# Kernel optimization log

Measured on AMD Instinct MI355X. Metric: run time of the kernel, lower is better.

Reference implementation:

```python
import jax, jax.numpy as jnp
import numpy as np

NUM_FIELDS = 40
EMBED_DIM = 64
ATTN_DIM = 32

def _triu_index(n):
    i, j = np.triu_indices(n, k=1)
    return jnp.asarray(i, jnp.int32), jnp.asarray(j, jnp.int32)

def setup_inputs() -> dict:
    key = jax.random.key(0)
    k0, k1, k2, k3, k4, k5 = jax.random.split(key, 6)
    B = 8192
    inputs = jax.random.normal(k0, (B, NUM_FIELDS, EMBED_DIM), dtype=jnp.float32)
    # attention MLP params (PyTorch Linear default init scale ~ 1/sqrt(fan_in))
    s1 = 1.0 / np.sqrt(EMBED_DIM)
    s2 = 1.0 / np.sqrt(ATTN_DIM)
    W1 = jax.random.uniform(k1, (EMBED_DIM, ATTN_DIM), jnp.float32, -s1, s1)
    b1 = jax.random.uniform(k2, (ATTN_DIM,), jnp.float32, -s1, s1)
    w2 = jax.random.uniform(k3, (ATTN_DIM,), jnp.float32, -s2, s2)
    p = jax.random.uniform(k4, (EMBED_DIM,), jnp.float32, -s1, s1)
    return {"inputs": inputs, "W1": W1, "b1": b1, "w2": w2, "p": p}

def reference(inputs, W1, b1, w2, p):
    idx0, idx1 = _triu_index(NUM_FIELDS)  # [P], P = 780 pairs
    # gather pairwise field embeddings and take elementwise product: [B, P, D]
    prod = inputs[:, idx0, :] * inputs[:, idx1, :]
    # tiny attention MLP: Linear -> ReLU -> Linear(no bias) -> softmax over pairs
    h = jax.nn.relu(jnp.einsum('bpd,da->bpa', prod, W1) + b1)  # [B, P, A]
    logits = jnp.einsum('bpa,a->bp', h, w2)                    # [B, P]
    attn = jax.nn.softmax(logits, axis=1)                      # softmax over pair dim
    # attention-weighted sum pooling over pairs: [B, D]
    pooled = jnp.einsum('bp,bpd->bd', attn, prod)
    # final linear projection to scalar (dropout=0 / eval -> identity)
    return jnp.einsum('bd,d->b', pooled, p)
```

## Files before the change

### kernel.cpp

```cpp
#include <hip/hip_runtime.h>


typedef _Float16 f16;
typedef f16 f16x2 __attribute__((ext_vector_type(2)));
typedef f16 f16x4 __attribute__((ext_vector_type(4)));
typedef f16 f16x8 __attribute__((ext_vector_type(8)));
typedef float fx16 __attribute__((ext_vector_type(16)));

#define NF 40
#define NB 8192
#define STR 76

union V8 { f16x8 v8; f16x4 v4[2]; f16x2 v2[4]; };

__global__ __launch_bounds__(256, 4) void afm_kernel(
    const float* __restrict__ x,
    const float* __restrict__ W1,
    const float* __restrict__ b1,
    const float* __restrict__ w2,
    const float* __restrict__ p,
    float* __restrict__ out)
{
    __shared__ f16 xh[4][NF * STR];

    const int tid  = threadIdx.x;
    const int wid  = tid >> 6;
    const int lane = tid & 63;
    const int b    = blockIdx.x * 4 + wid;

    f16* Xs = &xh[wid][0];

    const float4* xb = (const float4*)(x + (size_t)b * (NF * 64));
#pragma unroll
    for (int t = 0; t < 5; ++t) {
        int g = t * 64 + lane;
        float4 v0 = xb[g * 2];
        float4 v1 = xb[g * 2 + 1];
        f16x4 lo = { (f16)v0.x, (f16)v0.y, (f16)v0.z, (f16)v0.w };
        f16x4 hi = { (f16)v1.x, (f16)v1.y, (f16)v1.z, (f16)v1.w };
        int row = g >> 3, gg = g & 7;
        f16* dst = Xs + row * STR + gg * 8;
        *(f16x4*)dst = lo;
        *(f16x4*)(dst + 4) = hi;
    }

    const int nl = lane & 31;
    const int hh = lane >> 5;
    const int h8 = hh * 8;

    f16x8 w1f[4];
#pragma unroll
    for (int kt = 0; kt < 4; ++kt)
#pragma unroll
        for (int j = 0; j < 8; ++j)
            w1f[kt][j] = (f16)W1[(kt * 16 + h8 + j) * 32 + nl];

    f16x2 pp[16];
#pragma unroll
    for (int kt = 0; kt < 4; ++kt)
#pragma unroll
        for (int m = 0; m < 4; ++m) {
            f16x2 t2 = { (f16)p[kt * 16 + h8 + 2 * m], (f16)p[kt * 16 + h8 + 2 * m + 1] };
            pp[kt * 4 + m] = t2;
        }

    fx16 b1C;
    f16x2 w2h[8];
#pragma unroll
    for (int r = 0; r < 16; ++r) {
        int a = (r & 3) + 8 * (r >> 2) + 4 * hh;
        b1C[r] = b1[a];
    }
#pragma unroll
    for (int m = 0; m < 8; ++m) {
        int r = 2 * m;
        int a = (r & 3) + 8 * (r >> 2) + 4 * hh;
        f16x2 t2 = { (f16)(w2[a] * 1.44269504f), (f16)(w2[a + 1] * 1.44269504f) };
        w2h[m] = t2;
    }

    f16x4 xif[8];
    {
        const f16* src = Xs + nl * STR + h8;
#pragma unroll
        for (int kt = 0; kt < 4; ++kt) {
            xif[2 * kt]     = *(const f16x4*)(src + kt * 16);
            xif[2 * kt + 1] = *(const f16x4*)(src + kt * 16 + 4);
        }
    }

    float accW = 0.f, accWS = 0.f;

    auto body = [&](const f16x4* xi, int jrow, bool valid) {
        const f16* base = Xs + jrow * STR + h8;
        V8 pr[4];
#pragma unroll
        for (int kt = 0; kt < 4; ++kt) {
            f16x4 a0 = *(const f16x4*)(base + kt * 16);
            f16x4 a1 = *(const f16x4*)(base + kt * 16 + 4);
            pr[kt].v4[0] = xi[2 * kt] * a0;
            pr[kt].v4[1] = xi[2 * kt + 1] * a1;
        }
        fx16 C = __builtin_amdgcn_mfma_f32_32x32x16_f16(w1f[0], pr[0].v8, b1C, 0, 0, 0);
        C = __builtin_amdgcn_mfma_f32_32x32x16_f16(w1f[1], pr[1].v8, C, 0, 0, 0);
        C = __builtin_amdgcn_mfma_f32_32x32x16_f16(w1f[2], pr[2].v8, C, 0, 0, 0);
        C = __builtin_amdgcn_mfma_f32_32x32x16_f16(w1f[3], pr[3].v8, C, 0, 0, 0);
        float s0 = 0.f, s1 = 0.f, s2 = 0.f, s3 = 0.f;
#pragma unroll
        for (int m = 0; m < 4; ++m) {
            s0 = __builtin_amdgcn_fdot2(pr[0].v2[m], pp[m],      s0, false);
            s1 = __builtin_amdgcn_fdot2(pr[1].v2[m], pp[4 + m],  s1, false);
            s2 = __builtin_amdgcn_fdot2(pr[2].v2[m], pp[8 + m],  s2, false);
            s3 = __builtin_amdgcn_fdot2(pr[3].v2[m], pp[12 + m], s3, false);
        }
        float sp = (s0 + s1) + (s2 + s3);
        const f16x2 z2 = { (f16)0.f, (f16)0.f };
        float l0 = 0.f, l1 = 0.f;
#pragma unroll
        for (int m = 0; m < 8; ++m) {
            f16x2 hm = __builtin_bit_cast(f16x2,
                __builtin_amdgcn_cvt_pkrtz(C[2 * m], C[2 * m + 1]));
            hm = __builtin_elementwise_max(hm, z2);
            if (m & 1) l1 = __builtin_amdgcn_fdot2(hm, w2h[m], l1, false);
            else       l0 = __builtin_amdgcn_fdot2(hm, w2h[m], l0, false);
        }
        float l = l0 + l1;
        l  += __shfl_xor(l, 32);
        sp += __shfl_xor(sp, 32);
        float w = __builtin_amdgcn_exp2f(l);
        if (!valid) w = 0.f;
        accW += w;
        accWS = fmaf(w, sp, accWS);
    };

    for (int t = 1; t <= 24; ++t) {
        int jrow = (t <= 16) ? ((nl + t) & 31) : (t + 15);
        bool valid = (t != 16) || (nl < 16);
        body(xif, jrow, valid);
    }
    {
        int q = nl < 28 ? nl : 27;
        float disc = 225.0f - 8.0f * (float)q;
        int ii = (int)((15.0f - sqrtf(disc)) * 0.5f);
        if (ii * (15 - ii) / 2 > q) --ii;
        if ((ii + 1) * (14 - ii) / 2 <= q) ++ii;
        int jj = q - ii * (15 - ii) / 2 + ii + 1;
        int iC = 32 + ii, jC = 32 + jj;
        f16x4 xi2[8];
        const f16* src = Xs + iC * STR + h8;
#pragma unroll
        for (int kt = 0; kt < 4; ++kt) {
            xi2[2 * kt]     = *(const f16x4*)(src + kt * 16);
            xi2[2 * kt + 1] = *(const f16x4*)(src + kt * 16 + 4);
        }
        body(xi2, jC, nl < 28);
    }

#pragma unroll
    for (int m = 16; m >= 1; m >>= 1) {
        accW  += __shfl_xor(accW, m);
        accWS += __shfl_xor(accWS, m);
    }
    if (lane == 0) out[b] = accWS / accW;
}

extern "C" void kernel_launch(void* const* d_in, const int* in_sizes, int n_in,
                              void* d_out, int out_size, void* d_ws, size_t ws_size,
                              hipStream_t stream) {
    const float* x  = (const float*)d_in[0];
    const float* W1 = (const float*)d_in[1];
    const float* b1 = (const float*)d_in[2];
    const float* w2 = (const float*)d_in[3];
    const float* p  = (const float*)d_in[4];
    float* out = (float*)d_out;
    dim3 grid(NB / 4), block(256);
    hipLaunchKernelGGL(afm_kernel, grid, block, 0, stream, x, W1, b1, w2, p, out);
}
```

Measured before the change: 150.1 us.

## Split MFMA accumulation chain, pre-scale xi by p, defer sp shuffle

```diff
diff --git a/kernel.cpp b/kernel.cpp
--- a/kernel.cpp
+++ b/kernel.cpp
@@ -55,21 +55,12 @@
         for (int j = 0; j < 8; ++j)
             w1f[kt][j] = (f16)W1[(kt * 16 + h8 + j) * 32 + nl];
 
-    f16x2 pp[16];
-#pragma unroll
-    for (int kt = 0; kt < 4; ++kt)
-#pragma unroll
-        for (int m = 0; m < 4; ++m) {
-            f16x2 t2 = { (f16)p[kt * 16 + h8 + 2 * m], (f16)p[kt * 16 + h8 + 2 * m + 1] };
-            pp[kt * 4 + m] = t2;
-        }
-
-    fx16 b1C;
+    fx16 b1h;
     f16x2 w2h[8];
 #pragma unroll
     for (int r = 0; r < 16; ++r) {
         int a = (r & 3) + 8 * (r >> 2) + 4 * hh;
-        b1C[r] = b1[a];
+        b1h[r] = 0.5f * b1[a];
     }
 #pragma unroll
     for (int m = 0; m < 8; ++m) {
@@ -88,45 +79,54 @@
             xif[2 * kt + 1] = *(const f16x4*)(src + kt * 16 + 4);
         }
     }
+    f16x2 xip[16];
+#pragma unroll
+    for (int kt = 0; kt < 4; ++kt) {
+        V8 u; u.v4[0] = xif[2 * kt]; u.v4[1] = xif[2 * kt + 1];
+#pragma unroll
+        for (int m = 0; m < 4; ++m) {
+            f16x2 pe = { (f16)p[kt * 16 + h8 + 2 * m], (f16)p[kt * 16 + h8 + 2 * m + 1] };
+            xip[kt * 4 + m] = u.v2[m] * pe;
+        }
+    }
 
     float accW = 0.f, accWS = 0.f;
 
-    auto body = [&](const f16x4* xi, int jrow, bool valid) {
+    auto body = [&](const f16x4* xi, const f16x2* xp, int jrow, bool valid) {
         const f16* base = Xs + jrow * STR + h8;
-        V8 pr[4];
+        float s[4];
+        fx16 Ca, Cb;
 #pragma unroll
         for (int kt = 0; kt < 4; ++kt) {
-            f16x4 a0 = *(const f16x4*)(base + kt * 16);
-            f16x4 a1 = *(const f16x4*)(base + kt * 16 + 4);
-            pr[kt].v4[0] = xi[2 * kt] * a0;
-            pr[kt].v4[1] = xi[2 * kt + 1] * a1;
+            V8 xj;
+            xj.v4[0] = *(const f16x4*)(base + kt * 16);
+            xj.v4[1] = *(const f16x4*)(base + kt * 16 + 4);
+            float sk = 0.f;
+#pragma unroll
+            for (int m = 0; m < 4; ++m)
+                sk = __builtin_amdgcn_fdot2(xj.v2[m], xp[kt * 4 + m], sk, false);
+            s[kt] = sk;
+            V8 pr;
+            pr.v4[0] = xi[2 * kt] * xj.v4[0];
+            pr.v4[1] = xi[2 * kt + 1] * xj.v4[1];
+            if (kt == 0)      Ca = __builtin_amdgcn_mfma_f32_32x32x16_f16(w1f[0], pr.v8, b1h, 0, 0, 0);
+            else if (kt == 1) Ca = __builtin_amdgcn_mfma_f32_32x32x16_f16(w1f[1], pr.v8, Ca,  0, 0, 0);
+            else if (kt == 2) Cb = __builtin_amdgcn_mfma_f32_32x32x16_f16(w1f[2], pr.v8, b1h, 0, 0, 0);
+            else              Cb = __builtin_amdgcn_mfma_f32_32x32x16_f16(w1f[3], pr.v8, Cb,  0, 0, 0);
         }
-        fx16 C = __builtin_amdgcn_mfma_f32_32x32x16_f16(w1f[0], pr[0].v8, b1C, 0, 0, 0);
-        C = __builtin_amdgcn_mfma_f32_32x32x16_f16(w1f[1], pr[1].v8, C, 0, 0, 0);
-        C = __builtin_amdgcn_mfma_f32_32x32x16_f16(w1f[2], pr[2].v8, C, 0, 0, 0);
-        C = __builtin_amdgcn_mfma_f32_32x32x16_f16(w1f[3], pr[3].v8, C, 0, 0, 0);
-        float s0 = 0.f, s1 = 0.f, s2 = 0.f, s3 = 0.f;
-#pragma unroll
-        for (int m = 0; m < 4; ++m) {
-            s0 = __builtin_amdgcn_fdot2(pr[0].v2[m], pp[m],      s0, false);
-            s1 = __builtin_amdgcn_fdot2(pr[1].v2[m], pp[4 + m],  s1, false);
-            s2 = __builtin_amdgcn_fdot2(pr[2].v2[m], pp[8 + m],  s2, false);
-            s3 = __builtin_amdgcn_fdot2(pr[3].v2[m], pp[12 + m], s3, false);
-        }
-        float sp = (s0 + s1) + (s2 + s3);
+        float sp = (s[0] + s[1]) + (s[2] + s[3]);
+        fx16 Cs = Ca + Cb;
         const f16x2 z2 = { (f16)0.f, (f16)0.f };
-        float l0 = 0.f, l1 = 0.f;
+        float la[4] = { 0.f, 0.f, 0.f, 0.f };
 #pragma unroll
         for (int m = 0; m < 8; ++m) {
             f16x2 hm = __builtin_bit_cast(f16x2,
-                __builtin_amdgcn_cvt_pkrtz(C[2 * m], C[2 * m + 1]));
+                __builtin_amdgcn_cvt_pkrtz(Cs[2 * m], Cs[2 * m + 1]));
             hm = __builtin_elementwise_max(hm, z2);
-            if (m & 1) l1 = __builtin_amdgcn_fdot2(hm, w2h[m], l1, false);
-            else       l0 = __builtin_amdgcn_fdot2(hm, w2h[m], l0, false);
+            la[m & 3] = __builtin_amdgcn_fdot2(hm, w2h[m], la[m & 3], false);
         }
-        float l = l0 + l1;
-        l  += __shfl_xor(l, 32);
-        sp += __shfl_xor(sp, 32);
+        float l = (la[0] + la[1]) + (la[2] + la[3]);
+        l += __shfl_xor(l, 32);
         float w = __builtin_amdgcn_exp2f(l);
         if (!valid) w = 0.f;
         accW += w;
@@ -136,7 +136,7 @@
     for (int t = 1; t <= 24; ++t) {
         int jrow = (t <= 16) ? ((nl + t) & 31) : (t + 15);
         bool valid = (t != 16) || (nl < 16);
-        body(xif, jrow, valid);
+        body(xif, xip, jrow, valid);
     }
     {
         int q = nl < 28 ? nl : 27;
@@ -153,9 +153,20 @@
             xi2[2 * kt]     = *(const f16x4*)(src + kt * 16);
             xi2[2 * kt + 1] = *(const f16x4*)(src + kt * 16 + 4);
         }
-        body(xi2, jC, nl < 28);
+        f16x2 xip2[16];
+#pragma unroll
+        for (int kt = 0; kt < 4; ++kt) {
+            V8 u; u.v4[0] = xi2[2 * kt]; u.v4[1] = xi2[2 * kt + 1];
+#pragma unroll
+            for (int m = 0; m < 4; ++m) {
+                f16x2 pe = { (f16)p[kt * 16 + h8 + 2 * m], (f16)p[kt * 16 + h8 + 2 * m + 1] };
+                xip2[kt * 4 + m] = u.v2[m] * pe;
+            }
+        }
+        body(xi2, xip2, jC, nl < 28);
     }
 
+    accWS += __shfl_xor(accWS, 32);
 #pragma unroll
     for (int m = 16; m >= 1; m >>= 1) {
         accW  += __shfl_xor(accW, m);
```

Result: slower. 173.6 us (+15.6%).
